# Kernel tuning notes

Hardware: AMD Instinct MI355X
Metric: run time of the kernel (lower is better)

The kernel has to match this reference:

```python
import jax, jax.numpy as jnp
import numpy as np

DIM = 1024      # internal_dim
HEADS = 16
HD = DIM // HEADS
M = 256         # meaning_dim (protected prefix)
E = 4           # num_experts
K = 2           # top_k
HID = 2048      # dim * ffn_mult
MID = 2048      # DeepNarrow mid = 2*dim
LB = 0.01
EPS = 1.1920929e-07  # torch.finfo(float32).eps (nn.RMSNorm default)


def _rms(x, w):
    return x * jax.lax.rsqrt(jnp.mean(x * x, axis=-1, keepdims=True) + EPS) * w


def _gelu(x):
    return jax.nn.gelu(x, approximate=False)  # F.gelu default (erf)


def setup_inputs() -> dict:
    key = jax.random.key(0)
    ks = jax.random.split(key, 20)
    d = DIM
    w = lambda k, s: (jax.random.normal(k, s, jnp.float32) * 0.02)
    return {
        "x": jax.random.normal(ks[0], (4, 1024, d), jnp.float32),
        "n1_w": jnp.ones((d,), jnp.float32),
        "n2_w": jnp.ones((d,), jnp.float32),
        "wq": w(ks[1], (d, d)), "wk": w(ks[2], (d, d)),
        "wv": w(ks[3], (d, d)), "wo": w(ks[4], (d, d)),
        "qn_w": jnp.ones((HD,), jnp.float32), "kn_w": jnp.ones((HD,), jnp.float32),
        "gate_w": w(ks[5], (E, d)),
        # expert 0: StandardFFN
        "e0_up": w(ks[6], (HID, d)), "e0_down": w(ks[7], (d, HID)),
        # expert 1: SwiGLUFFN
        "e1_w1": w(ks[8], (HID, d)), "e1_w2": w(ks[9], (HID, d)), "e1_down": w(ks[10], (d, HID)),
        # expert 2: DeepNarrowFFN
        "e2_l1": w(ks[11], (MID, d)), "e2_l2": w(ks[12], (HID, MID)),
        "e2_l3": w(ks[13], (MID, HID)), "e2_l4": w(ks[14], (d, MID)),
        # expert 3: BottleneckFFN (neck = dim)
        "e3_down": w(ks[15], (d, d)), "e3_up": w(ks[16], (HID, d)), "e3_out": w(ks[17], (d, HID)),
    }


def reference(x, n1_w, n2_w, wq, wk, wv, wo, qn_w, kn_w, gate_w,
              e0_up, e0_down, e1_w1, e1_w2, e1_down,
              e2_l1, e2_l2, e2_l3, e2_l4, e3_down, e3_up, e3_out):
    B, T, C = x.shape
    # ---- attention with QK-norm, causal (NoPE) ----
    h = _rms(x, n1_w)
    heads = lambda w_: (h @ w_.T).reshape(B, T, HEADS, HD).transpose(0, 2, 1, 3)  # [B,H,T,hd]
    q = _rms(heads(wq), qn_w)
    k = _rms(heads(wk), kn_w)
    v = heads(wv)
    scores = jnp.einsum('bhqd,bhkd->bhqk', q, k) * (HD ** -0.5)
    causal = jnp.tril(jnp.ones((T, T), bool))
    scores = jnp.where(causal[None, None], scores, -jnp.inf)
    attn = jax.nn.softmax(scores, axis=-1)
    ao = jnp.einsum('bhqk,bhkd->bhqd', attn, v).transpose(0, 2, 1, 3).reshape(B, T, C) @ wo.T
    ao = ao.at[:, :, :M].set(0.0)  # protect meaning dims
    x = x + ao
    # ---- heterogeneous MoE, top-k routing ----
    xf = _rms(x, n2_w).reshape(-1, C)  # [N,C]
    N = xf.shape[0]
    logits = jnp.nan_to_num(xf @ gate_w.T)
    probs = jax.nn.softmax(logits, axis=-1)
    topv, topi = jax.lax.top_k(probs, K)
    topv = topv / (topv.sum(-1, keepdims=True) + 1e-8)
    # dense per-token combine weights: zero for unselected experts (same math as dispatch loop)
    wts = jnp.zeros((N, E), x.dtype).at[jnp.arange(N)[:, None], topi].add(topv)
    o0 = _gelu(xf @ e0_up.T) @ e0_down.T
    o1 = (jax.nn.silu(xf @ e1_w1.T) * (xf @ e1_w2.T)) @ e1_down.T
    o2 = _gelu(_gelu(_gelu(xf @ e2_l1.T) @ e2_l2.T) @ e2_l3.T) @ e2_l4.T
    o3 = _gelu(_gelu(xf @ e3_down.T) @ e3_up.T) @ e3_out.T
    moe = (wts[:, 0:1] * o0 + wts[:, 1:2] * o1 + wts[:, 2:3] * o2 + wts[:, 3:4] * o3)
    moe = moe.reshape(B, T, C).at[:, :, :M].set(0.0)
    return x + moe
```

## Files before the change

kernel.cpp:

```cpp
#include <hip/hip_runtime.h>
#include <math.h>

#define DIM   1024
#define NTOK  4096
#define TSEQ  1024
#define NHEAD 16
#define MPROT 256
#define EPSR  1.1920929e-07f
#define SA    64.0f
#define SW    256.0f
#define SPC   64.0f
#define MAXI  160

typedef __attribute__((ext_vector_type(8))) short          short8;
typedef __attribute__((ext_vector_type(8))) _Float16       half8;
typedef __attribute__((ext_vector_type(4))) _Float16       half4;
typedef __attribute__((ext_vector_type(4))) float          f32x4;
typedef __attribute__((ext_vector_type(4))) unsigned short us4;

static __device__ __forceinline__ float bf2f(unsigned short s) {
  union { unsigned int u; float f; } c; c.u = ((unsigned int)s) << 16; return c.f;
}
static __device__ __forceinline__ unsigned short f2bf(float f) {
  union { float f; unsigned int u; } c; c.f = f;
  return (unsigned short)((c.u + 0x7fffu + ((c.u >> 16) & 1u)) >> 16);
}
static __device__ __forceinline__ void gload16(void* lds, const void* g) {
  __builtin_amdgcn_global_load_lds(
      (__attribute__((address_space(1))) void*)const_cast<void*>(g),
      (__attribute__((address_space(3))) void*)lds, 16, 0, 0);
}

static __device__ __forceinline__ void tile_swz(int& m0, int& n0) {
  const int gx = gridDim.x;
  const int L = blockIdx.y * gx + blockIdx.x;
  const int xcd = L & 7;
  const int j = L >> 3;
  const int mbq = j / gx;
  const int nb = j - mbq * gx;
  m0 = ((mbq << 3) | xcd) << 7;
  n0 = nb << 7;
}

__global__ __launch_bounds__(256) void cvt_attn4_k(const float* __restrict__ wq,
                                                   const float* __restrict__ wk,
                                                   const float* __restrict__ wv,
                                                   const float* __restrict__ wo,
                                                   _Float16* __restrict__ dh,
                                                   _Float16* __restrict__ dl) {
  const int wi = blockIdx.y;
  const float* s = (wi == 0) ? wq : (wi == 1) ? wk : (wi == 2) ? wv : wo;
  const int i = blockIdx.x * 256 + threadIdx.x;
  const size_t off4 = ((size_t)wi << 20) >> 2;
  const float4 v = ((const float4*)s)[i];
  float a0 = v.x * SW, a1 = v.y * SW, a2 = v.z * SW, a3 = v.w * SW;
  half4 hv, lv;
  _Float16 h0 = (_Float16)a0; hv[0] = h0; lv[0] = (_Float16)(a0 - (float)h0);
  _Float16 h1 = (_Float16)a1; hv[1] = h1; lv[1] = (_Float16)(a1 - (float)h1);
  _Float16 h2 = (_Float16)a2; hv[2] = h2; lv[2] = (_Float16)(a2 - (float)h2);
  _Float16 h3 = (_Float16)a3; hv[3] = h3; lv[3] = (_Float16)(a3 - (float)h3);
  ((half4*)dh)[off4 + i] = hv; ((half4*)dl)[off4 + i] = lv;
}

__global__ __launch_bounds__(256) void cvt_moe_all_k(
    const float* s0, const float* s1, const float* s2, const float* s3,
    const float* s4, const float* s5, const float* s6, const float* s7,
    const float* s8, const float* s9, const float* s10, const float* s11,
    unsigned short* __restrict__ dst) {
  const int n4tab[12] = {524288, 524288, 524288, 524288, 524288, 524288,
                         1048576, 1048576, 524288, 262144, 524288, 524288};
  const size_t offtab[12] = {0, 2097152, 4194304, 6291456, 8388608, 10485760,
                             12582912, 16777216, 20971520, 23068672, 24117248, 26214400};
  const int wi = blockIdx.y;
  const int i = blockIdx.x * 256 + threadIdx.x;
  if (i >= n4tab[wi]) return;
  const float* s;
  switch (wi) {
    case 0: s = s0; break; case 1: s = s1; break; case 2: s = s2; break;
    case 3: s = s3; break; case 4: s = s4; break; case 5: s = s5; break;
    case 6: s = s6; break; case 7: s = s7; break; case 8: s = s8; break;
    case 9: s = s9; break; case 10: s = s10; break; default: s = s11; break;
  }
  const float4 v = ((const float4*)s)[i];
  us4 o; o[0] = f2bf(v.x); o[1] = f2bf(v.y); o[2] = f2bf(v.z); o[3] = f2bf(v.w);
  ((us4*)(dst + offtab[wi]))[i] = o;
}

__global__ __launch_bounds__(256) void rms_split_k(const float* __restrict__ in,
                                                   const float* __restrict__ wgt,
                                                   _Float16* __restrict__ oh,
                                                   _Float16* __restrict__ ol) {
  const int row = blockIdx.x, tid = threadIdx.x;
  const float4 v = ((const float4*)(in + (size_t)row * DIM))[tid];
  float ss = v.x * v.x + v.y * v.y + v.z * v.z + v.w * v.w;
#pragma unroll
  for (int o = 32; o; o >>= 1) ss += __shfl_xor(ss, o);
  __shared__ float red[4];
  if ((tid & 63) == 0) red[tid >> 6] = ss;
  __syncthreads();
  const float sc = rsqrtf((red[0] + red[1] + red[2] + red[3]) * (1.0f / DIM) + EPSR) * SA;
  const float4 wv = ((const float4*)wgt)[tid];
  float a[4] = {v.x * sc * wv.x, v.y * sc * wv.y, v.z * sc * wv.z, v.w * sc * wv.w};
  half4 hv, lv;
#pragma unroll
  for (int j = 0; j < 4; ++j) {
    _Float16 hh = (_Float16)a[j]; hv[j] = hh; lv[j] = (_Float16)(a[j] - (float)hh);
  }
  ((half4*)(oh + (size_t)row * DIM))[tid] = hv;
  ((half4*)(ol + (size_t)row * DIM))[tid] = lv;
}

__global__ __launch_bounds__(256) void rmsgate_k(const float* __restrict__ x2,
                                                 const float* __restrict__ n2w,
                                                 const float* __restrict__ gw,
                                                 unsigned short* __restrict__ xfb,
                                                 float* __restrict__ wts,
                                                 float* __restrict__ moe) {
  const int row = blockIdx.x, tid = threadIdx.x;
  ((float4*)(moe + (size_t)row * DIM))[tid] = (float4){0.f, 0.f, 0.f, 0.f};
  const float4 v = ((const float4*)(x2 + (size_t)row * DIM))[tid];
  float ss = v.x * v.x + v.y * v.y + v.z * v.z + v.w * v.w;
#pragma unroll
  for (int o = 32; o; o >>= 1) ss += __shfl_xor(ss, o);
  __shared__ float red[4];
  __shared__ float redE[4][4];
  const int w = tid >> 6, lane = tid & 63;
  if (lane == 0) red[w] = ss;
  __syncthreads();
  const float sc = rsqrtf((red[0] + red[1] + red[2] + red[3]) * (1.0f / DIM) + EPSR);
  const float4 nw = ((const float4*)n2w)[tid];
  const float xn0 = v.x * sc * nw.x, xn1 = v.y * sc * nw.y;
  const float xn2 = v.z * sc * nw.z, xn3 = v.w * sc * nw.w;
  us4 ob; ob[0] = f2bf(xn0); ob[1] = f2bf(xn1); ob[2] = f2bf(xn2); ob[3] = f2bf(xn3);
  ((us4*)(xfb + (size_t)row * DIM))[tid] = ob;
#pragma unroll
  for (int e = 0; e < 4; ++e) {
    const float4 g = ((const float4*)(gw + (size_t)e * DIM))[tid];
    float d = xn0 * g.x + xn1 * g.y + xn2 * g.z + xn3 * g.w;
#pragma unroll
    for (int o = 32; o; o >>= 1) d += __shfl_xor(d, o);
    if (lane == 0) redE[w][e] = d;
  }
  __syncthreads();
  if (tid == 0) {
    float lg[4];
#pragma unroll
    for (int e = 0; e < 4; ++e) lg[e] = redE[0][e] + redE[1][e] + redE[2][e] + redE[3][e];
    const float mx = fmaxf(fmaxf(lg[0], lg[1]), fmaxf(lg[2], lg[3]));
    float pe[4]; float sum = 0.0f;
#pragma unroll
    for (int e = 0; e < 4; ++e) { pe[e] = __expf(lg[e] - mx); sum += pe[e]; }
#pragma unroll
    for (int e = 0; e < 4; ++e) pe[e] /= sum;
    int i1 = 0;
    for (int e = 1; e < 4; ++e) if (pe[e] > pe[i1]) i1 = e;
    int i2 = -1;
    for (int e = 0; e < 4; ++e) { if (e == i1) continue; if (i2 < 0 || pe[e] > pe[i2]) i2 = e; }
    const float s2 = pe[i1] + pe[i2] + 1e-8f;
    float o[4] = {0.f, 0.f, 0.f, 0.f};
    o[i1] = pe[i1] / s2; o[i2] = pe[i2] / s2;
    float4 r; r.x = o[0]; r.y = o[1]; r.z = o[2]; r.w = o[3];
    *(float4*)(wts + (size_t)row * 4) = r;
  }
}

__global__ __launch_bounds__(256) void qknorm2_k(_Float16* __restrict__ qh,
                                                 _Float16* __restrict__ ql,
                                                 _Float16* __restrict__ kh,
                                                 _Float16* __restrict__ kl,
                                                 const float* __restrict__ qnw,
                                                 const float* __restrict__ knw) {
  _Float16* ph; _Float16* pl; const float* wgt;
  if (blockIdx.y == 0) { ph = qh; pl = ql; wgt = qnw; }
  else { ph = kh; pl = kl; wgt = knw; }
  const int idx = (blockIdx.x << 2) + (threadIdx.x >> 6);
  const int lane = threadIdx.x & 63;
  const size_t off = ((size_t)idx << 6) + lane;
  const float v = (float)ph[off] + (float)pl[off];
  float ss = v * v;
#pragma unroll
  for (int o = 32; o; o >>= 1) ss += __shfl_xor(ss, o);
  const float sc = rsqrtf(ss * (1.0f / (64.0f * SA * SA)) + EPSR);
  const float nv = v * sc * wgt[lane];
  _Float16 hh = (_Float16)nv;
  ph[off] = hh; pl[off] = (_Float16)(nv - (float)hh);
}

struct MoeCfg { int nbn[4][4]; int ks[4][4]; };

__global__ __launch_bounds__(256) void route2_k(const float* __restrict__ wts,
                                                int* __restrict__ idxP,
                                                int* __restrict__ meta,
                                                int* __restrict__ work,
                                                MoeCfg cfg) {
  const int tid = threadIdx.x, w = tid >> 6, lane = tid & 63;
  __shared__ int wsum[4];
  __shared__ int baseS;
  int off = 0;
  for (int e = 0; e < 4; ++e) {
    if (tid == 0) baseS = 0;
    __syncthreads();
    for (int c = 0; c < 16; ++c) {
      const int tok = (c << 8) + tid;
      const bool pred = wts[(size_t)tok * 4 + e] > 0.0f;
      const unsigned long long m = __ballot(pred);
      const int lanepre = __popcll(m & ((1ull << lane) - 1ull));
      if (lane == 0) wsum[w] = __popcll(m);
      __syncthreads();
      int wpre = 0;
#pragma unroll
      for (int i = 0; i < 4; ++i) wpre += (i < w) ? wsum[i] : 0;
      const int tot = wsum[0] + wsum[1] + wsum[2] + wsum[3];
      if (pred) idxP[off + baseS + wpre + lanepre] = tok;
      __syncthreads();
      if (tid == 0) baseS += tot;
      __syncthreads();
    }
    const int cnt = baseS;
    const int padded = (cnt + 127) & ~127;
    for (int j = cnt + tid; j < padded; j += 256) idxP[off + j] = -1;
    if (tid == 0) meta[80 + e] = off;
    const int mb0 = off >> 7, nmb = padded >> 7;
    for (int j = tid; j < nmb; j += 256) meta[mb0 + j] = e;
    off += padded;
    __syncthreads();
  }
  for (int j = (off >> 7) + tid; j < 72; j += 256) meta[j] = -1;
  for (int j = tid; j < 4 * 8 * MAXI; j += 256) work[j] = -1;
  __syncthreads();
  if (tid < 32) {
    const int p = tid >> 3, x = tid & 7;
    int* wb = work + p * (8 * MAXI);
    int n = 0;
    const int totmb = off >> 7;
    for (int mb = x; mb < totmb; mb += 8) {
      const int e = meta[mb];
      const int nbn = cfg.nbn[p][e];
      const int ks = cfg.ks[p][e];
      for (int nb = 0; nb < nbn; ++nb)
        for (int k = 0; k < ks; ++k) {
          wb[n * 8 + x] = mb | (nb << 8) | (k << 16);
          ++n;
        }
    }
  }
}

struct SubOpP {
  const unsigned short* A;
  const unsigned short* Bw;
  unsigned short* outb;
  const unsigned short* other;
  int K, nbn, act, ep, gath, ks;
};
struct PhaseP { SubOpP op[4]; };

__global__ __launch_bounds__(256, 4) void gemm_moe_k(PhaseP ph,
                                                     const int* __restrict__ meta,
                                                     const int* __restrict__ idxP,
                                                     const float* __restrict__ wts,
                                                     float* __restrict__ moe,
                                                     const int* __restrict__ wk) {
  __shared__ unsigned short As[128][64];
  __shared__ unsigned short Bs[128][64];
  const int item = wk[blockIdx.y * 8 + blockIdx.x];
  if (item < 0) return;
  const int mb = item & 255;
  const int nb = (item >> 8) & 255;
  const int kpart = (item >> 16) & 3;
  const int e = meta[mb];
  SubOpP op;
  switch (e) {
    case 0: op = ph.op[0]; break;
    case 1: op = ph.op[1]; break;
    case 2: op = ph.op[2]; break;
    default: op = ph.op[3]; break;
  }
  const int m0p = mb << 7;
  const int lr0 = m0p - meta[80 + e];
  const int n0 = nb << 7;
  const int F = op.nbn << 7;
  const int K = op.K;
  const int tid = threadIdx.x;
  const int w = tid >> 6, lane = tid & 63;
  const int wr = ((w >> 1) << 6), wc = ((w & 1) << 6);
  const int rr = lane & 15, kgl = lane >> 4;
  const int srow = tid >> 3, sslot = tid & 7;

  int grow[4];
#pragma unroll
  for (int i = 0; i < 4; ++i) {
    const int r = (i << 5) + srow;
    if (op.gath) {
      const int t = idxP[m0p + r];
      grow[i] = (t < 0) ? 0 : t;
    } else {
      grow[i] = lr0 + r;
    }
  }

  f32x4 acc[4][4];
#pragma unroll
  for (int a_ = 0; a_ < 4; ++a_)
#pragma unroll
    for (int b_ = 0; b_ < 4; ++b_) acc[a_][b_] = (f32x4){0.f, 0.f, 0.f, 0.f};

  int kt0 = 0, ktN = K >> 6;
  if (op.ks == 2) { const int hgt = ktN >> 1; kt0 = kpart * hgt; ktN = kt0 + hgt; }
  for (int kt = kt0; kt < ktN; ++kt) {
    const int k0 = kt << 6;
#pragma unroll
    for (int i = 0; i < 4; ++i) {
      const int r = (i << 5) + srow;
      const int ls = sslot ^ (r & 7);
      gload16(&As[(i << 5) + (w << 3)][0], op.A + (size_t)grow[i] * K + k0 + (ls << 3));
      gload16(&Bs[(i << 5) + (w << 3)][0], op.Bw + (size_t)(n0 + r) * K + k0 + (ls << 3));
    }
    __syncthreads();
    short8 af[4][2], bfr[4][2];
#pragma unroll
    for (int f = 0; f < 4; ++f) {
#pragma unroll
      for (int ks = 0; ks < 2; ++ks) {
        const int row = wr + (f << 4) + rr;
        const int kg = (ks << 2) + kgl;
        af[f][ks] = *(const short8*)&As[row][(kg ^ (row & 7)) << 3];
        const int col = wc + (f << 4) + rr;
        bfr[f][ks] = *(const short8*)&Bs[col][(kg ^ (col & 7)) << 3];
      }
    }
#pragma unroll
    for (int fi = 0; fi < 4; ++fi)
#pragma unroll
      for (int fj = 0; fj < 4; ++fj)
#pragma unroll
        for (int ks = 0; ks < 2; ++ks)
          acc[fi][fj] = __builtin_amdgcn_mfma_f32_16x16x32_bf16(
              af[fi][ks], bfr[fj][ks], acc[fi][fj], 0, 0, 0);
    __syncthreads();
  }
#pragma unroll
  for (int fi = 0; fi < 4; ++fi)
#pragma unroll
    for (int fj = 0; fj < 4; ++fj) {
      const int col = n0 + wc + (fj << 4) + rr;
#pragma unroll
      for (int r = 0; r < 4; ++r) {
        const int rl = wr + (fi << 4) + (kgl << 2) + r;
        float v = acc[fi][fj][r];
        if (op.act) v = 0.5f * v * (1.0f + erff(v * 0.70710678118654752f));
        if (op.ep == 0) {
          op.outb[(size_t)(lr0 + rl) * F + col] = f2bf(v);
        } else if (op.ep == 1) {
          const size_t off = (size_t)(lr0 + rl) * F + col;
          const float sv = v / (1.0f + __expf(-v));
          op.outb[off] = f2bf(sv * bf2f(op.other[off]));
        } else {
          const int tok = idxP[m0p + rl];
          if (tok >= 0)
            atomicAdd(&moe[(size_t)tok * DIM + col], wts[(size_t)tok * 4 + e] * v);
        }
      }
    }
}

template <int EP>
__global__ __launch_bounds__(256, 4) void gemm_split_k(
    const _Float16* __restrict__ Ah, const _Float16* __restrict__ Al,
    const _Float16* __restrict__ Bh, const _Float16* __restrict__ Bl,
    int K, int F,
    _Float16* __restrict__ Oh, _Float16* __restrict__ Ol, float oscale,
    const float* __restrict__ resid, float* __restrict__ outf,
    _Float16* __restrict__ K2h, _Float16* __restrict__ K2l,
    _Float16* __restrict__ V2h, _Float16* __restrict__ V2l) {
  __shared__ _Float16 AsH[128][32], AsL[128][32];
  __shared__ _Float16 BsH[128][32], BsL[128][32];
  const int tid = threadIdx.x;
  const int w = tid >> 6, lane = tid & 63;
  const int wr = ((w >> 1) << 6), wc = ((w & 1) << 6);
  int m0, n0;
  tile_swz(m0, n0);
  const int rr = lane & 15, kgl = lane >> 4;
  const int srow = tid >> 2, sslot = tid & 3;

  f32x4 acc[4][4];
#pragma unroll
  for (int a_ = 0; a_ < 4; ++a_)
#pragma unroll
    for (int b_ = 0; b_ < 4; ++b_) acc[a_][b_] = (f32x4){0.f, 0.f, 0.f, 0.f};

  const int KT = K >> 5;
  for (int kt = 0; kt < KT; ++kt) {
    const int k0 = kt << 5;
#pragma unroll
    for (int i = 0; i < 2; ++i) {
      const int r = (i << 6) + srow;
      const int ls = sslot ^ ((r >> 1) & 3);
      const size_t ga = (size_t)(m0 + r) * K + k0 + (ls << 3);
      const size_t gb = (size_t)(n0 + r) * K + k0 + (ls << 3);
      const int lr = (i << 6) + (w << 4);
      gload16(&AsH[lr][0], Ah + ga);
      gload16(&AsL[lr][0], Al + ga);
      gload16(&BsH[lr][0], Bh + gb);
      gload16(&BsL[lr][0], Bl + gb);
    }
    __syncthreads();
    half8 ah[4], al[4], bh[4], bl[4];
#pragma unroll
    for (int f = 0; f < 4; ++f) {
      const int row = wr + (f << 4) + rr;
      const int pa = (kgl ^ ((row >> 1) & 3)) << 3;
      ah[f] = *(const half8*)&AsH[row][pa];
      al[f] = *(const half8*)&AsL[row][pa];
      const int col = wc + (f << 4) + rr;
      const int pb = (kgl ^ ((col >> 1) & 3)) << 3;
      bh[f] = *(const half8*)&BsH[col][pb];
      bl[f] = *(const half8*)&BsL[col][pb];
    }
#pragma unroll
    for (int fi = 0; fi < 4; ++fi)
#pragma unroll
      for (int fj = 0; fj < 4; ++fj) {
        acc[fi][fj] = __builtin_amdgcn_mfma_f32_16x16x32_f16(ah[fi], bh[fj], acc[fi][fj], 0, 0, 0);
        acc[fi][fj] = __builtin_amdgcn_mfma_f32_16x16x32_f16(ah[fi], bl[fj], acc[fi][fj], 0, 0, 0);
        acc[fi][fj] = __builtin_amdgcn_mfma_f32_16x16x32_f16(al[fi], bh[fj], acc[fi][fj], 0, 0, 0);
      }
    __syncthreads();
  }
#pragma unroll
  for (int fi = 0; fi < 4; ++fi)
#pragma unroll
    for (int fj = 0; fj < 4; ++fj) {
      const int col = n0 + wc + (fj << 4) + rr;
      const int rowb = m0 + wr + (fi << 4) + (kgl << 2);
      if (EP == 3) {
        if (col < 2048) {
          _Float16* ph = (col < 1024) ? Oh : K2h;
          _Float16* pl = (col < 1024) ? Ol : K2l;
          const int c = col & 1023;
#pragma unroll
          for (int r = 0; r < 4; ++r) {
            const float v = acc[fi][fj][r] * oscale;
            const _Float16 hh2 = (_Float16)v;
            const size_t off = (size_t)(rowb + r) * DIM + c;
            ph[off] = hh2; pl[off] = (_Float16)(v - (float)hh2);
          }
        } else {
          const int c2 = col - 2048;
          half4 h4, l4;
#pragma unroll
          for (int r = 0; r < 4; ++r) {
            const float v = acc[fi][fj][r] * oscale;
            const _Float16 hh2 = (_Float16)v;
            h4[r] = hh2; l4[r] = (_Float16)(v - (float)hh2);
          }
          const size_t vt = ((size_t)((rowb >> 10) << 4) + (size_t)(c2 >> 6)) * 65536 +
                            (size_t)(c2 & 63) * 1024 + (size_t)(rowb & 1023);
          *(half4*)&V2h[vt] = h4;
          *(half4*)&V2l[vt] = l4;
        }
      } else {
#pragma unroll
        for (int r = 0; r < 4; ++r) {
          const size_t off = (size_t)(rowb + r) * F + col;
          const float v = acc[fi][fj][r] * oscale;
          outf[off] = resid[off] + (col >= MPROT ? v : 0.0f);
        }
      }
    }
}

__global__ __launch_bounds__(256, 2) void attn_k(
    const _Float16* __restrict__ Qh, const _Float16* __restrict__ Ql,
    const _Float16* __restrict__ Kh, const _Float16* __restrict__ Kl,
    const _Float16* __restrict__ Vth, const _Float16* __restrict__ Vtl,
    _Float16* __restrict__ Oh, _Float16* __restrict__ Ol) {
  __shared__ _Float16 Ksh[2][32][64], Ksl[2][32][64];
  __shared__ _Float16 Vsh[2][64][40], Vsl[2][64][40];
  __shared__ _Float16 Plh[4][16][40], Pll[4][16][40];
  const int n = blockIdx.x;
  const int qt = n >> 6;
  const int bh = ((n & 7) << 3) | ((n >> 3) & 7);
  const int b = bh >> 4, h = bh & 15;
  const int tid = threadIdx.x, w = tid >> 6, lane = tid & 63;
  const int rr = lane & 15, rg = lane >> 4;
  const size_t tokbase = (size_t)b * TSEQ;
  const int hcol = h << 6;
  const size_t vtbase = (size_t)bh << 16;
  const int q0w = (qt << 7) + (w << 5);
  const float sscale = 0.125f / (SA * SA);

  half8 qfh[2][2], qfl[2][2];
#pragma unroll
  for (int qf = 0; qf < 2; ++qf)
#pragma unroll
    for (int ks = 0; ks < 2; ++ks) {
      const size_t off = (tokbase + q0w + (qf << 4) + rr) * DIM + hcol + (ks << 5) + (rg << 3);
      qfh[qf][ks] = *(const half8*)&Qh[off];
      qfl[qf][ks] = *(const half8*)&Ql[off];
    }

  f32x4 oacc[2][4];
#pragma unroll
  for (int qf = 0; qf < 2; ++qf)
#pragma unroll
    for (int dg = 0; dg < 4; ++dg) oacc[qf][dg] = (f32x4){0.f, 0.f, 0.f, 0.f};
  float mreg[2] = {-INFINITY, -INFINITY}, lreg[2] = {0.f, 0.f};

  const int kr = (w << 3) + (lane >> 3);
  const int kswz = ((lane & 7) ^ (kr & 7)) << 3;
  const int vr = tid >> 2;
  const int vs = (tid & 3) << 3;

  const int ntiles = (qt + 1) << 2;

  {
    gload16(&Ksh[0][w << 3][0], &Kh[(tokbase + kr) * DIM + hcol + kswz]);
    gload16(&Ksl[0][w << 3][0], &Kl[(tokbase + kr) * DIM + hcol + kswz]);
    const half8 vvh = *(const half8*)&Vth[vtbase + (size_t)vr * TSEQ + vs];
    const half8 vvl = *(const half8*)&Vtl[vtbase + (size_t)vr * TSEQ + vs];
    *(half8*)&Vsh[0][vr][vs] = vvh;
    *(half8*)&Vsl[0][vr][vs] = vvl;
    __syncthreads();
  }

  for (int t = 0; t < ntiles; ++t) {
    const int cur = t & 1;
    const int kv0 = t << 5;
    const bool havenext = (t + 1 < ntiles);
    half8 nvh, nvl;
    if (havenext) {
      const int kn = kv0 + 32;
      gload16(&Ksh[cur ^ 1][w << 3][0], &Kh[(tokbase + kn + kr) * DIM + hcol + kswz]);
      gload16(&Ksl[cur ^ 1][w << 3][0], &Kl[(tokbase + kn + kr) * DIM + hcol + kswz]);
      nvh = *(const half8*)&Vth[vtbase + (size_t)vr * TSEQ + kn + vs];
      nvl = *(const half8*)&Vtl[vtbase + (size_t)vr * TSEQ + kn + vs];
    }
    if (kv0 <= q0w + 31) {
      half8 kfh[2][2], kfl[2][2];
#pragma unroll
      for (int kt = 0; kt < 2; ++kt)
#pragma unroll
        for (int ks = 0; ks < 2; ++ks) {
          const int row = (kt << 4) + rr;
          const int sw = ((((ks << 2) + rg)) ^ (row & 7)) << 3;
          kfh[kt][ks] = *(const half8*)&Ksh[cur][row][sw];
          kfl[kt][ks] = *(const half8*)&Ksl[cur][row][sw];
        }
#pragma unroll
      for (int qf = 0; qf < 2; ++qf) {
        if (kv0 > q0w + (qf << 4) + 15) continue;
        f32x4 st[2];
        st[0] = (f32x4){0.f, 0.f, 0.f, 0.f};
        st[1] = (f32x4){0.f, 0.f, 0.f, 0.f};
#pragma unroll
        for (int kt = 0; kt < 2; ++kt)
#pragma unroll
          for (int ks = 0; ks < 2; ++ks) {
            st[kt] = __builtin_amdgcn_mfma_f32_16x16x32_f16(kfh[kt][ks], qfh[qf][ks], st[kt], 0, 0, 0);
            st[kt] = __builtin_amdgcn_mfma_f32_16x16x32_f16(kfh[kt][ks], qfl[qf][ks], st[kt], 0, 0, 0);
            st[kt] = __builtin_amdgcn_mfma_f32_16x16x32_f16(kfl[kt][ks], qfh[qf][ks], st[kt], 0, 0, 0);
          }
        const int qg = q0w + (qf << 4) + rr;
        float s[2][4]; float mx = -INFINITY;
#pragma unroll
        for (int kt = 0; kt < 2; ++kt)
#pragma unroll
          for (int r = 0; r < 4; ++r) {
            float sv = st[kt][r] * sscale;
            if (kv0 + (kt << 4) + (rg << 2) + r > qg) sv = -INFINITY;
            s[kt][r] = sv; mx = fmaxf(mx, sv);
          }
        mx = fmaxf(mx, __shfl_xor(mx, 16));
        mx = fmaxf(mx, __shfl_xor(mx, 32));
        const float mn = fmaxf(mreg[qf], mx);
        const float al = __expf(mreg[qf] - mn);
        mreg[qf] = mn;
        float p[2][4]; float rs = 0.f;
#pragma unroll
        for (int kt = 0; kt < 2; ++kt)
#pragma unroll
          for (int r = 0; r < 4; ++r) { p[kt][r] = __expf(s[kt][r] - mn); rs += p[kt][r]; }
        rs += __shfl_xor(rs, 16);
        rs += __shfl_xor(rs, 32);
        lreg[qf] = lreg[qf] * al + rs;
#pragma unroll
        for (int kt = 0; kt < 2; ++kt) {
          half4 h4, l4;
#pragma unroll
          for (int r = 0; r < 4; ++r) {
            const float pv = p[kt][r] * SPC;
            const _Float16 ph = (_Float16)pv;
            h4[r] = ph; l4[r] = (_Float16)(pv - (float)ph);
          }
          *(half4*)&Plh[w][rr][(kt << 4) + (rg << 2)] = h4;
          *(half4*)&Pll[w][rr][(kt << 4) + (rg << 2)] = l4;
        }
        float alr[4];
#pragma unroll
        for (int r = 0; r < 4; ++r) alr[r] = __shfl(al, (lane & 48) | ((rg << 2) + r));
#pragma unroll
        for (int dg = 0; dg < 4; ++dg)
#pragma unroll
          for (int r = 0; r < 4; ++r) oacc[qf][dg][r] *= alr[r];
        const half8 pah = *(const half8*)&Plh[w][rr][rg << 3];
        const half8 pal = *(const half8*)&Pll[w][rr][rg << 3];
#pragma unroll
        for (int dg = 0; dg < 4; ++dg) {
          const half8 vfh2 = *(const half8*)&Vsh[cur][(dg << 4) + rr][rg << 3];
          const half8 vfl2 = *(const half8*)&Vsl[cur][(dg << 4) + rr][rg << 3];
          oacc[qf][dg] = __builtin_amdgcn_mfma_f32_16x16x32_f16(pah, vfh2, oacc[qf][dg], 0, 0, 0);
          oacc[qf][dg] = __builtin_amdgcn_mfma_f32_16x16x32_f16(pah, vfl2, oacc[qf][dg], 0, 0, 0);
          oacc[qf][dg] = __builtin_amdgcn_mfma_f32_16x16x32_f16(pal, vfh2, oacc[qf][dg], 0, 0, 0);
        }
      }
    }
    if (havenext) {
      *(half8*)&Vsh[cur ^ 1][vr][vs] = nvh;
      *(half8*)&Vsl[cur ^ 1][vr][vs] = nvl;
    }
    __syncthreads();
  }
#pragma unroll
  for (int qf = 0; qf < 2; ++qf) {
    float li[4];
#pragma unroll
    for (int r = 0; r < 4; ++r)
      li[r] = __shfl(lreg[qf], (lane & 48) | ((rg << 2) + r));
#pragma unroll
    for (int dg = 0; dg < 4; ++dg)
#pragma unroll
      for (int r = 0; r < 4; ++r) {
        const int qloc = (rg << 2) + r;
        const float ov = oacc[qf][dg][r] / (li[r] * SPC);
        const _Float16 hh2 = (_Float16)ov;
        const size_t off = (tokbase + q0w + (qf << 4) + qloc) * DIM + hcol + (dg << 4) + rr;
        Oh[off] = hh2;
        Ol[off] = (_Float16)(ov - (float)hh2);
      }
  }
}

__global__ __launch_bounds__(256) void comb_k(float* __restrict__ outp,
                                              const float* __restrict__ moe) {
  const size_t i = (size_t)blockIdx.x * 256 + threadIdx.x;
  const int c4 = (int)(i & 255);
  if (c4 >= 64) {
    float4 o = ((float4*)outp)[i];
    const float4 m = ((const float4*)moe)[i];
    o.x += m.x; o.y += m.y; o.z += m.z; o.w += m.w;
    ((float4*)outp)[i] = o;
  }
}

extern "C" void kernel_launch(void* const* d_in, const int* in_sizes, int n_in,
                              void* d_out, int out_size, void* d_ws, size_t ws_size,
                              hipStream_t stream) {
  (void)in_sizes; (void)n_in; (void)out_size; (void)ws_size;
  const float* x    = (const float*)d_in[0];
  const float* n1w  = (const float*)d_in[1];
  const float* n2w  = (const float*)d_in[2];
  const float* wq   = (const float*)d_in[3];
  const float* wk   = (const float*)d_in[4];
  const float* wv   = (const float*)d_in[5];
  const float* wo   = (const float*)d_in[6];
  const float* qnw  = (const float*)d_in[7];
  const float* knw  = (const float*)d_in[8];
  const float* gw   = (const float*)d_in[9];
  const float* moesrc[12] = {
    (const float*)d_in[10], (const float*)d_in[11],
    (const float*)d_in[12], (const float*)d_in[13], (const float*)d_in[14],
    (const float*)d_in[15], (const float*)d_in[16], (const float*)d_in[17], (const float*)d_in[18],
    (const float*)d_in[19], (const float*)d_in[20], (const float*)d_in[21]
  };
  float* outp = (float*)d_out;

  char* p = (char*)d_ws;
  auto alloc = [&](size_t bytes) { void* r = (void*)p; p += (bytes + 255) & ~(size_t)255; return r; };
  const size_t NC = (size_t)NTOK * DIM;
  _Float16* hh = (_Float16*)alloc(NC * 2);
  _Float16* hl = (_Float16*)alloc(NC * 2);
  _Float16* qh = (_Float16*)alloc(NC * 2);
  _Float16* ql = (_Float16*)alloc(NC * 2);
  _Float16* kh = (_Float16*)alloc(NC * 2);
  _Float16* kl = (_Float16*)alloc(NC * 2);
  _Float16* vth = (_Float16*)alloc(NC * 2);
  _Float16* vtl = (_Float16*)alloc(NC * 2);
  unsigned short* xfb = (unsigned short*)alloc(NC * 2);
  float* moe = (float*)alloc(NC * 4);
  float* wts = (float*)alloc((size_t)NTOK * 4 * 4);
  _Float16* awh = (_Float16*)alloc((size_t)4 * 1024 * 1024 * 2);
  _Float16* awl = (_Float16*)alloc((size_t)4 * 1024 * 1024 * 2);
  unsigned short* moeW = (unsigned short*)alloc((size_t)28311552 * 2);
  int* idxP = (int*)alloc((size_t)9216 * 4);
  int* meta = (int*)alloc(512);
  int* work = (int*)alloc((size_t)4 * 8 * MAXI * 4);
  unsigned short* e0t = (unsigned short*)qh;
  unsigned short* e1a = (unsigned short*)kh;
  unsigned short* e2a = (unsigned short*)vth;
  unsigned short* e1b = (unsigned short*)alloc((size_t)NTOK * 2048 * 2);
  unsigned short* e2b = (unsigned short*)alloc((size_t)NTOK * 2048 * 2);
  unsigned short* e3a = (unsigned short*)alloc((size_t)NTOK * 1024 * 2);
  unsigned short* e3b = (unsigned short*)alloc((size_t)NTOK * 2048 * 2);
  unsigned short* e2c = e2a;

  const size_t moff[12] = {0, 2097152, 4194304, 6291456, 8388608, 10485760,
                           12582912, 16777216, 20971520, 23068672, 24117248, 26214400};
  auto mw = [&](int i) -> const unsigned short* { return moeW + moff[i]; };

  cvt_attn4_k<<<dim3(1024, 4), dim3(256), 0, stream>>>(wq, wk, wv, wo, awh, awl);
  cvt_moe_all_k<<<dim3(4096, 12), dim3(256), 0, stream>>>(
      moesrc[0], moesrc[1], moesrc[2], moesrc[3], moesrc[4], moesrc[5],
      moesrc[6], moesrc[7], moesrc[8], moesrc[9], moesrc[10], moesrc[11], moeW);
  const _Float16* woh = awh + (3 << 20); const _Float16* wol = awl + (3 << 20);

  rms_split_k<<<dim3(NTOK), dim3(256), 0, stream>>>(x, n1w, hh, hl);
  gemm_split_k<3><<<dim3(24, 32), dim3(256), 0, stream>>>(
      hh, hl, awh, awl, 1024, 3072, qh, ql, 1.0f / SW, nullptr, nullptr,
      kh, kl, vth, vtl);
  qknorm2_k<<<dim3(NTOK * NHEAD / 4, 2), dim3(256), 0, stream>>>(qh, ql, kh, kl, qnw, knw);
  attn_k<<<dim3(512), dim3(256), 0, stream>>>(qh, ql, kh, kl, vth, vtl, hh, hl);
  gemm_split_k<1><<<dim3(8, 32), dim3(256), 0, stream>>>(
      hh, hl, woh, wol, 1024, 1024, nullptr, nullptr, 1.0f / (SA * SW), x, outp,
      nullptr, nullptr, nullptr, nullptr);

  rmsgate_k<<<dim3(NTOK), dim3(256), 0, stream>>>(outp, n2w, gw, xfb, wts, moe);

  MoeCfg cfg;
  const int nbn_tab[4][4] = {{16, 16, 16, 8},
                             {8, 16, 16, 16},
                             {0, 8, 16, 8},
                             {0, 0, 8, 0}};
  const int ks_tab[4][4]  = {{1, 1, 1, 1},
                             {2, 1, 1, 1},
                             {1, 2, 1, 2},
                             {1, 1, 2, 1}};
  for (int pp = 0; pp < 4; ++pp)
    for (int ee = 0; ee < 4; ++ee) { cfg.nbn[pp][ee] = nbn_tab[pp][ee]; cfg.ks[pp][ee] = ks_tab[pp][ee]; }

  route2_k<<<dim3(1), dim3(256), 0, stream>>>(wts, idxP, meta, work, cfg);

  auto mk = [&](const unsigned short* A, const unsigned short* B, unsigned short* outb,
                const unsigned short* other, int K, int nbn, int act, int ep, int gath, int ks) {
    SubOpP s; s.A = A; s.Bw = B; s.outb = outb; s.other = other;
    s.K = K; s.nbn = nbn; s.act = act; s.ep = ep; s.gath = gath; s.ks = ks;
    return s;
  };
  const SubOpP none = mk(nullptr, nullptr, nullptr, nullptr, 1024, 0, 0, 0, 0, 1);

  PhaseP p1;
  p1.op[0] = mk(xfb, mw(0), e0t, nullptr, 1024, 16, 1, 0, 1, 1);
  p1.op[1] = mk(xfb, mw(3), e1a, nullptr, 1024, 16, 0, 0, 1, 1);
  p1.op[2] = mk(xfb, mw(5), e2a, nullptr, 1024, 16, 1, 0, 1, 1);
  p1.op[3] = mk(xfb, mw(9), e3a, nullptr, 1024, 8, 1, 0, 1, 1);
  gemm_moe_k<<<dim3(8, MAXI), dim3(256), 0, stream>>>(p1, meta, idxP, wts, moe, work);

  PhaseP p2;
  p2.op[0] = mk(e0t, mw(1), nullptr, nullptr, 2048, 8, 0, 2, 0, 2);
  p2.op[1] = mk(xfb, mw(2), e1b, e1a, 1024, 16, 0, 1, 1, 1);
  p2.op[2] = mk(e2a, mw(6), e2b, nullptr, 2048, 16, 1, 0, 0, 1);
  p2.op[3] = mk(e3a, mw(10), e3b, nullptr, 1024, 16, 1, 0, 0, 1);
  gemm_moe_k<<<dim3(8, MAXI), dim3(256), 0, stream>>>(p2, meta, idxP, wts, moe, work + 8 * MAXI);

  PhaseP p3;
  p3.op[0] = none;
  p3.op[1] = mk(e1b, mw(4), nullptr, nullptr, 2048, 8, 0, 2, 0, 2);
  p3.op[2] = mk(e2b, mw(7), e2c, nullptr, 2048, 16, 1, 0, 0, 1);
  p3.op[3] = mk(e3b, mw(11), nullptr, nullptr, 2048, 8, 0, 2, 0, 2);
  gemm_moe_k<<<dim3(8, MAXI), dim3(256), 0, stream>>>(p3, meta, idxP, wts, moe, work + 16 * MAXI);

  PhaseP p4;
  p4.op[0] = none;
  p4.op[1] = none;
  p4.op[2] = mk(e2c, mw(8), nullptr, nullptr, 2048, 8, 0, 2, 0, 2);
  p4.op[3] = none;
  gemm_moe_k<<<dim3(8, MAXI), dim3(256), 0, stream>>>(p4, meta, idxP, wts, moe, work + 24 * MAXI);

  comb_k<<<dim3(4096), dim3(256), 0, stream>>>(outp, moe);
}
```

Measured before the change: 633.7 us.

## Fuse QK-norm into QKV GEMM, atomically accumulate MoE into output, rebalance phases

Moves the per-head Q/K RMSNorm into the QKV GEMM epilogue using lane shuffles, which removes a separate read-modify-write kernel. MoE down-projections now atomically add straight into the residual output and skip protected columns, so the moe buffer, its zeroing and the combine kernel go away. Expert 3's final projection moves from phase 3 to phase 4 to balance the phase workloads. The attention kernel pairs causal q-tiles from both ends to balance blocks and raises wave priority around its MFMA sections.

```diff
diff --git a/kernel.cpp b/kernel.cpp
--- a/kernel.cpp
+++ b/kernel.cpp
@@ -114,10 +114,8 @@
                                                  const float* __restrict__ n2w,
                                                  const float* __restrict__ gw,
                                                  unsigned short* __restrict__ xfb,
-                                                 float* __restrict__ wts,
-                                                 float* __restrict__ moe) {
+                                                 float* __restrict__ wts) {
   const int row = blockIdx.x, tid = threadIdx.x;
-  ((float4*)(moe + (size_t)row * DIM))[tid] = (float4){0.f, 0.f, 0.f, 0.f};
   const float4 v = ((const float4*)(x2 + (size_t)row * DIM))[tid];
   float ss = v.x * v.x + v.y * v.y + v.z * v.z + v.w * v.w;
 #pragma unroll
@@ -162,28 +160,6 @@
     float4 r; r.x = o[0]; r.y = o[1]; r.z = o[2]; r.w = o[3];
     *(float4*)(wts + (size_t)row * 4) = r;
   }
-}
-
-__global__ __launch_bounds__(256) void qknorm2_k(_Float16* __restrict__ qh,
-                                                 _Float16* __restrict__ ql,
-                                                 _Float16* __restrict__ kh,
-                                                 _Float16* __restrict__ kl,
-                                                 const float* __restrict__ qnw,
-                                                 const float* __restrict__ knw) {
-  _Float16* ph; _Float16* pl; const float* wgt;
-  if (blockIdx.y == 0) { ph = qh; pl = ql; wgt = qnw; }
-  else { ph = kh; pl = kl; wgt = knw; }
-  const int idx = (blockIdx.x << 2) + (threadIdx.x >> 6);
-  const int lane = threadIdx.x & 63;
-  const size_t off = ((size_t)idx << 6) + lane;
-  const float v = (float)ph[off] + (float)pl[off];
-  float ss = v * v;
-#pragma unroll
-  for (int o = 32; o; o >>= 1) ss += __shfl_xor(ss, o);
-  const float sc = rsqrtf(ss * (1.0f / (64.0f * SA * SA)) + EPSR);
-  const float nv = v * sc * wgt[lane];
-  _Float16 hh = (_Float16)nv;
-  ph[off] = hh; pl[off] = (_Float16)(nv - (float)hh);
 }
 
 struct MoeCfg { int nbn[4][4]; int ks[4][4]; };
@@ -259,7 +235,7 @@
                                                      const int* __restrict__ meta,
                                                      const int* __restrict__ idxP,
                                                      const float* __restrict__ wts,
-                                                     float* __restrict__ moe,
+                                                     float* __restrict__ outp,
                                                      const int* __restrict__ wk) {
   __shared__ unsigned short As[128][64];
   __shared__ unsigned short Bs[128][64];
@@ -357,8 +333,8 @@
           op.outb[off] = f2bf(sv * bf2f(op.other[off]));
         } else {
           const int tok = idxP[m0p + rl];
-          if (tok >= 0)
-            atomicAdd(&moe[(size_t)tok * DIM + col], wts[(size_t)tok * 4 + e] * v);
+          if (tok >= 0 && col >= MPROT)
+            atomicAdd(&outp[(size_t)tok * DIM + col], wts[(size_t)tok * 4 + e] * v);
         }
       }
     }
@@ -372,7 +348,8 @@
     _Float16* __restrict__ Oh, _Float16* __restrict__ Ol, float oscale,
     const float* __restrict__ resid, float* __restrict__ outf,
     _Float16* __restrict__ K2h, _Float16* __restrict__ K2l,
-    _Float16* __restrict__ V2h, _Float16* __restrict__ V2l) {
+    _Float16* __restrict__ V2h, _Float16* __restrict__ V2l,
+    const float* __restrict__ qnw, const float* __restrict__ knw) {
   __shared__ _Float16 AsH[128][32], AsL[128][32];
   __shared__ _Float16 BsH[128][32], BsL[128][32];
   const int tid = threadIdx.x;
@@ -427,6 +404,44 @@
       }
     __syncthreads();
   }
+
+  if (EP == 3 && n0 < 2048) {
+    const bool isq = (n0 < 1024);
+    _Float16* ph = isq ? Oh : K2h;
+    _Float16* pl = isq ? Ol : K2l;
+    const float* wvec = isq ? qnw : knw;
+    float wreg[4];
+#pragma unroll
+    for (int fj = 0; fj < 4; ++fj) wreg[fj] = wvec[(fj << 4) + rr];
+#pragma unroll
+    for (int fi = 0; fi < 4; ++fi) {
+#pragma unroll
+      for (int r = 0; r < 4; ++r) {
+        float vv[4]; float ss = 0.f;
+#pragma unroll
+        for (int fj = 0; fj < 4; ++fj) {
+          vv[fj] = acc[fi][fj][r] * oscale;
+          ss += vv[fj] * vv[fj];
+        }
+        ss += __shfl_xor(ss, 1);
+        ss += __shfl_xor(ss, 2);
+        ss += __shfl_xor(ss, 4);
+        ss += __shfl_xor(ss, 8);
+        const float sc = rsqrtf(ss * (1.0f / (64.0f * SA * SA)) + EPSR);
+        const int row = m0 + wr + (fi << 4) + (kgl << 2) + r;
+#pragma unroll
+        for (int fj = 0; fj < 4; ++fj) {
+          const int c = (n0 + wc + (fj << 4) + rr) & 1023;
+          const float nv = vv[fj] * sc * wreg[fj];
+          const _Float16 hh2 = (_Float16)nv;
+          const size_t off = (size_t)row * DIM + c;
+          ph[off] = hh2; pl[off] = (_Float16)(nv - (float)hh2);
+        }
+      }
+    }
+    return;
+  }
+
 #pragma unroll
   for (int fi = 0; fi < 4; ++fi)
 #pragma unroll
@@ -434,31 +449,18 @@
       const int col = n0 + wc + (fj << 4) + rr;
       const int rowb = m0 + wr + (fi << 4) + (kgl << 2);
       if (EP == 3) {
-        if (col < 2048) {
-          _Float16* ph = (col < 1024) ? Oh : K2h;
-          _Float16* pl = (col < 1024) ? Ol : K2l;
-          const int c = col & 1023;
-#pragma unroll
-          for (int r = 0; r < 4; ++r) {
-            const float v = acc[fi][fj][r] * oscale;
-            const _Float16 hh2 = (_Float16)v;
-            const size_t off = (size_t)(rowb + r) * DIM + c;
-            ph[off] = hh2; pl[off] = (_Float16)(v - (float)hh2);
-          }
-        } else {
-          const int c2 = col - 2048;
-          half4 h4, l4;
-#pragma unroll
-          for (int r = 0; r < 4; ++r) {
-            const float v = acc[fi][fj][r] * oscale;
-            const _Float16 hh2 = (_Float16)v;
-            h4[r] = hh2; l4[r] = (_Float16)(v - (float)hh2);
-          }
-          const size_t vt = ((size_t)((rowb >> 10) << 4) + (size_t)(c2 >> 6)) * 65536 +
-                            (size_t)(c2 & 63) * 1024 + (size_t)(rowb & 1023);
-          *(half4*)&V2h[vt] = h4;
-          *(half4*)&V2l[vt] = l4;
-        }
+        const int c2 = col - 2048;
+        half4 h4, l4;
+#pragma unroll
+        for (int r = 0; r < 4; ++r) {
+          const float v = acc[fi][fj][r] * oscale;
+          const _Float16 hh2 = (_Float16)v;
+          h4[r] = hh2; l4[r] = (_Float16)(v - (float)hh2);
+        }
+        const size_t vt = ((size_t)((rowb >> 10) << 4) + (size_t)(c2 >> 6)) * 65536 +
+                          (size_t)(c2 & 63) * 1024 + (size_t)(rowb & 1023);
+        *(half4*)&V2h[vt] = h4;
+        *(half4*)&V2l[vt] = l4;
       } else {
 #pragma unroll
         for (int r = 0; r < 4; ++r) {
@@ -479,8 +481,10 @@
   __shared__ _Float16 Vsh[2][64][40], Vsl[2][64][40];
   __shared__ _Float16 Plh[4][16][40], Pll[4][16][40];
   const int n = blockIdx.x;
-  const int qt = n >> 6;
-  const int bh = ((n & 7) << 3) | ((n >> 3) & 7);
+  const int j = n >> 1, s = n & 1;
+  const int pt = j >> 6;
+  const int qt = s ? (7 - pt) : pt;
+  const int bh = j & 63;
   const int b = bh >> 4, h = bh & 15;
   const int tid = threadIdx.x, w = tid >> 6, lane = tid & 63;
   const int rr = lane & 15, rg = lane >> 4;
@@ -553,6 +557,7 @@
         f32x4 st[2];
         st[0] = (f32x4){0.f, 0.f, 0.f, 0.f};
         st[1] = (f32x4){0.f, 0.f, 0.f, 0.f};
+        __builtin_amdgcn_s_setprio(1);
 #pragma unroll
         for (int kt = 0; kt < 2; ++kt)
 #pragma unroll
@@ -561,15 +566,16 @@
             st[kt] = __builtin_amdgcn_mfma_f32_16x16x32_f16(kfh[kt][ks], qfl[qf][ks], st[kt], 0, 0, 0);
             st[kt] = __builtin_amdgcn_mfma_f32_16x16x32_f16(kfl[kt][ks], qfh[qf][ks], st[kt], 0, 0, 0);
           }
+        __builtin_amdgcn_s_setprio(0);
         const int qg = q0w + (qf << 4) + rr;
-        float s[2][4]; float mx = -INFINITY;
+        float s2[2][4]; float mx = -INFINITY;
 #pragma unroll
         for (int kt = 0; kt < 2; ++kt)
 #pragma unroll
           for (int r = 0; r < 4; ++r) {
             float sv = st[kt][r] * sscale;
             if (kv0 + (kt << 4) + (rg << 2) + r > qg) sv = -INFINITY;
-            s[kt][r] = sv; mx = fmaxf(mx, sv);
+            s2[kt][r] = sv; mx = fmaxf(mx, sv);
           }
         mx = fmaxf(mx, __shfl_xor(mx, 16));
         mx = fmaxf(mx, __shfl_xor(mx, 32));
@@ -580,7 +586,7 @@
 #pragma unroll
         for (int kt = 0; kt < 2; ++kt)
 #pragma unroll
-          for (int r = 0; r < 4; ++r) { p[kt][r] = __expf(s[kt][r] - mn); rs += p[kt][r]; }
+          for (int r = 0; r < 4; ++r) { p[kt][r] = __expf(s2[kt][r] - mn); rs += p[kt][r]; }
         rs += __shfl_xor(rs, 16);
         rs += __shfl_xor(rs, 32);
         lreg[qf] = lreg[qf] * al + rs;
@@ -605,6 +611,7 @@
           for (int r = 0; r < 4; ++r) oacc[qf][dg][r] *= alr[r];
         const half8 pah = *(const half8*)&Plh[w][rr][rg << 3];
         const half8 pal = *(const half8*)&Pll[w][rr][rg << 3];
+        __builtin_amdgcn_s_setprio(1);
 #pragma unroll
         for (int dg = 0; dg < 4; ++dg) {
           const half8 vfh2 = *(const half8*)&Vsh[cur][(dg << 4) + rr][rg << 3];
@@ -613,6 +620,7 @@
           oacc[qf][dg] = __builtin_amdgcn_mfma_f32_16x16x32_f16(pah, vfl2, oacc[qf][dg], 0, 0, 0);
           oacc[qf][dg] = __builtin_amdgcn_mfma_f32_16x16x32_f16(pal, vfh2, oacc[qf][dg], 0, 0, 0);
         }
+        __builtin_amdgcn_s_setprio(0);
       }
     }
     if (havenext) {
@@ -638,18 +646,6 @@
         Oh[off] = hh2;
         Ol[off] = (_Float16)(ov - (float)hh2);
       }
-  }
-}
-
-__global__ __launch_bounds__(256) void comb_k(float* __restrict__ outp,
-                                              const float* __restrict__ moe) {
-  const size_t i = (size_t)blockIdx.x * 256 + threadIdx.x;
-  const int c4 = (int)(i & 255);
-  if (c4 >= 64) {
-    float4 o = ((float4*)outp)[i];
-    const float4 m = ((const float4*)moe)[i];
-    o.x += m.x; o.y += m.y; o.z += m.z; o.w += m.w;
-    ((float4*)outp)[i] = o;
   }
 }
 
@@ -687,7 +683,6 @@
   _Float16* vth = (_Float16*)alloc(NC * 2);
   _Float16* vtl = (_Float16*)alloc(NC * 2);
   unsigned short* xfb = (unsigned short*)alloc(NC * 2);
-  float* moe = (float*)alloc(NC * 4);
   float* wts = (float*)alloc((size_t)NTOK * 4 * 4);
   _Float16* awh = (_Float16*)alloc((size_t)4 * 1024 * 1024 * 2);
   _Float16* awl = (_Float16*)alloc((size_t)4 * 1024 * 1024 * 2);
@@ -717,24 +712,23 @@
   rms_split_k<<<dim3(NTOK), dim3(256), 0, stream>>>(x, n1w, hh, hl);
   gemm_split_k<3><<<dim3(24, 32), dim3(256), 0, stream>>>(
       hh, hl, awh, awl, 1024, 3072, qh, ql, 1.0f / SW, nullptr, nullptr,
-      kh, kl, vth, vtl);
-  qknorm2_k<<<dim3(NTOK * NHEAD / 4, 2), dim3(256), 0, stream>>>(qh, ql, kh, kl, qnw, knw);
+      kh, kl, vth, vtl, qnw, knw);
   attn_k<<<dim3(512), dim3(256), 0, stream>>>(qh, ql, kh, kl, vth, vtl, hh, hl);
   gemm_split_k<1><<<dim3(8, 32), dim3(256), 0, stream>>>(
       hh, hl, woh, wol, 1024, 1024, nullptr, nullptr, 1.0f / (SA * SW), x, outp,
-      nullptr, nullptr, nullptr, nullptr);
-
-  rmsgate_k<<<dim3(NTOK), dim3(256), 0, stream>>>(outp, n2w, gw, xfb, wts, moe);
+      nullptr, nullptr, nullptr, nullptr, nullptr, nullptr);
+
+  rmsgate_k<<<dim3(NTOK), dim3(256), 0, stream>>>(outp, n2w, gw, xfb, wts);
 
   MoeCfg cfg;
   const int nbn_tab[4][4] = {{16, 16, 16, 8},
                              {8, 16, 16, 16},
-                             {0, 8, 16, 8},
-                             {0, 0, 8, 0}};
+                             {0, 8, 16, 0},
+                             {0, 0, 8, 8}};
   const int ks_tab[4][4]  = {{1, 1, 1, 1},
                              {2, 1, 1, 1},
-                             {1, 2, 1, 2},
-                             {1, 1, 2, 1}};
+                             {1, 2, 1, 1},
+                             {1, 1, 2, 2}};
   for (int pp = 0; pp < 4; ++pp)
     for (int ee = 0; ee < 4; ++ee) { cfg.nbn[pp][ee] = nbn_tab[pp][ee]; cfg.ks[pp][ee] = ks_tab[pp][ee]; }
 
@@ -753,28 +747,26 @@
   p1.op[1] = mk(xfb, mw(3), e1a, nullptr, 1024, 16, 0, 0, 1, 1);
   p1.op[2] = mk(xfb, mw(5), e2a, nullptr, 1024, 16, 1, 0, 1, 1);
   p1.op[3] = mk(xfb, mw(9), e3a, nullptr, 1024, 8, 1, 0, 1, 1);
-  gemm_moe_k<<<dim3(8, MAXI), dim3(256), 0, stream>>>(p1, meta, idxP, wts, moe, work);
+  gemm_moe_k<<<dim3(8, MAXI), dim3(256), 0, stream>>>(p1, meta, idxP, wts, outp, work);
 
   PhaseP p2;
   p2.op[0] = mk(e0t, mw(1), nullptr, nullptr, 2048, 8, 0, 2, 0, 2);
   p2.op[1] = mk(xfb, mw(2), e1b, e1a, 1024, 16, 0, 1, 1, 1);
   p2.op[2] = mk(e2a, mw(6), e2b, nullptr, 2048, 16, 1, 0, 0, 1);
   p2.op[3] = mk(e3a, mw(10), e3b, nullptr, 1024, 16, 1, 0, 0, 1);
-  gemm_moe_k<<<dim3(8, MAXI), dim3(256), 0, stream>>>(p2, meta, idxP, wts, moe, work + 8 * MAXI);
+  gemm_moe_k<<<dim3(8, MAXI), dim3(256), 0, stream>>>(p2, meta, idxP, wts, outp, work + 8 * MAXI);
 
   PhaseP p3;
   p3.op[0] = none;
   p3.op[1] = mk(e1b, mw(4), nullptr, nullptr, 2048, 8, 0, 2, 0, 2);
   p3.op[2] = mk(e2b, mw(7), e2c, nullptr, 2048, 16, 1, 0, 0, 1);
-  p3.op[3] = mk(e3b, mw(11), nullptr, nullptr, 2048, 8, 0, 2, 0, 2);
-  gemm_moe_k<<<dim3(8, MAXI), dim3(256), 0, stream>>>(p3, meta, idxP, wts, moe, work + 16 * MAXI);
+  p3.op[3] = none;
+  gemm_moe_k<<<dim3(8, MAXI), dim3(256), 0, stream>>>(p3, meta, idxP, wts, outp, work + 16 * MAXI);
 
   PhaseP p4;
   p4.op[0] = none;
   p4.op[1] = none;
   p4.op[2] = mk(e2c, mw(8), nullptr, nullptr, 2048, 8, 0, 2, 0, 2);
-  p4.op[3] = none;
-  gemm_moe_k<<<dim3(8, MAXI), dim3(256), 0, stream>>>(p4, meta, idxP, wts, moe, work + 24 * MAXI);
-
-  comb_k<<<dim3(4096), dim3(256), 0, stream>>>(outp, moe);
-}
+  p4.op[3] = mk(e3b, mw(11), nullptr, nullptr, 2048, 8, 0, 2, 0, 2);
+  gemm_moe_k<<<dim3(8, MAXI), dim3(256), 0, stream>>>(p4, meta, idxP, wts, outp, work + 24 * MAXI);
+}
```

After: 596.3 us. -5.9%, faster.
